# Performance work log

Hardware: AMD Instinct MI355X
Metric: run time of the kernel (lower is better)

Reference implementation:

```python
import jax, jax.numpy as jnp
import numpy as np

EPS = 1e-8


def setup_inputs() -> dict:
    key = jax.random.key(0)
    k1, = jax.random.split(key, 1)
    B, C, T = 8, 512, 16000
    x = jax.random.normal(k1, (B, C, T), dtype=jnp.float32)
    gamma = jnp.ones((1, C, 1), dtype=jnp.float32)
    beta = jnp.zeros((1, C, 1), dtype=jnp.float32)
    return {"x": x, "gamma": gamma, "beta": beta}


def reference(x, gamma, beta):
    # x: [B, C, T] cumulative layer norm (cLN)
    B, C, T = x.shape
    counts = C * (jnp.arange(T, dtype=x.dtype) + 1.0)  # [T], elements seen so far
    counts = counts.reshape(1, 1, T)
    # cumulative mean over (channels x time-so-far)
    mean = jnp.cumsum(x.sum(axis=1, keepdims=True), axis=2) / counts  # [B,1,T]
    # cumulative variance of residuals w.r.t. running mean (as in original)
    var = jnp.cumsum(((x - mean) ** 2).sum(axis=1, keepdims=True), axis=2) / counts  # [B,1,T]
    return (x - mean) / jnp.sqrt(var + EPS) * gamma + beta
```

## Files before the change

### kernel.cpp

```cpp
#include <hip/hip_runtime.h>
#include <hip/hip_bf16.h>


constexpr int Bb = 8;
constexpr int Cc = 512;
constexpr int Tt = 16000;
constexpr int T4 = Tt / 4;
constexpr int TCH = 128;
constexpr int T4CH = TCH / 4;
constexpr int NCHK = Tt / TCH;
constexpr float EPSF = 1e-8f;

typedef float f32x4 __attribute__((ext_vector_type(4)));

__device__ __forceinline__ unsigned long long pack_av(float v) {
    return (1ull << 32) | (unsigned long long)__float_as_uint(v);
}

__device__ __forceinline__ float lookback_sum(const unsigned long long* W,
                                              int chain_base, int k, int lane)
{
    float carry = 0.f;
    #pragma unroll 1
    for (int base = 0; base < k; base += 64) {
        const int j = base + lane;
        float v = 0.f;
        if (j < k) {
            unsigned long long w;
            for (;;) {
                w = __hip_atomic_load(&W[chain_base + j], __ATOMIC_RELAXED,
                                      __HIP_MEMORY_SCOPE_AGENT);
                if (w >> 32) break;
                __builtin_amdgcn_s_sleep(1);
            }
            v = __uint_as_float((unsigned)w);
        }
        #pragma unroll
        for (int m = 1; m < 64; m <<= 1) v += __shfl_xor(v, m, 64);
        carry += v;
    }
    return carry;
}

__global__ __launch_bounds__(1024)
void fused_cln_kernel(const float* __restrict__ x,
                      const float* __restrict__ gamma,
                      const float* __restrict__ beta,
                      float* __restrict__ out,
                      unsigned long long* __restrict__ W1,
                      unsigned long long* __restrict__ W2)
{
    const int bid = blockIdx.x;
    const int k = bid >> 3;
    const int b = bid & 7;
    const int tid = threadIdx.x;
    const int c_sub = tid >> 5;
    const int t4s   = tid & 31;

    __shared__ float gam[Cc], bet[Cc];
    if (tid < Cc) { gam[tid] = gamma[tid]; bet[tid] = beta[tid]; }

    const f32x4* xb = (const f32x4*)x + ((size_t)(b * Cc + c_sub)) * T4 + k * T4CH + t4s;
    f32x4 xr[16];
    #pragma unroll
    for (int r = 0; r < 16; ++r) xr[r] = xb[(size_t)r * 32 * T4];

    f32x4 ps = 0, pq = 0;
    #pragma unroll
    for (int r = 0; r < 16; ++r) { ps += xr[r]; pq += xr[r] * xr[r]; }

    __shared__ f32x4 red_s[32][32];
    __shared__ f32x4 red_q[32][32];
    red_s[c_sub][t4s] = ps;
    red_q[c_sub][t4s] = pq;
    __syncthreads();
    #pragma unroll
    for (int s = 16; s > 0; s >>= 1) {
        if (c_sub < s) {
            red_s[c_sub][t4s] += red_s[c_sub + s][t4s];
            red_q[c_sub][t4s] += red_q[c_sub + s][t4s];
        }
        __syncthreads();
    }

    __shared__ f32x4 mean_l[32], istd_l[32];

    if (tid < 64) {
        const int lane = tid;
        const bool act = lane < 32;
        const int chain = b * NCHK;

        const f32x4 sv = act ? red_s[0][lane] : (f32x4)0.f;
        const f32x4 qv = act ? red_q[0][lane] : (f32x4)0.f;

        const float c0 = sv.x, c1 = c0 + sv.y, c2 = c1 + sv.z, c3 = c2 + sv.w;
        float lsum = act ? c3 : 0.f;
        float sc = lsum;
        #pragma unroll
        for (int off = 1; off < 64; off <<= 1) {
            const float n = __shfl_up(sc, off, 64);
            if (lane >= off) sc += n;
        }
        const float total1 = __shfl(sc, 63, 64);
        const float ex1 = sc - lsum;

        if (lane == 0)
            __hip_atomic_store(&W1[chain + k], pack_av(total1), __ATOMIC_RELAXED,
                               __HIP_MEMORY_SCOPE_AGENT);
        const float carry1 = lookback_sum(W1, chain, k, lane);

        const float t0f = (float)(k * TCH + lane * 4);
        f32x4 cnt;
        cnt.x = (float)Cc * (t0f + 1.f);
        cnt.y = (float)Cc * (t0f + 2.f);
        cnt.z = (float)Cc * (t0f + 3.f);
        cnt.w = (float)Cc * (t0f + 4.f);

        f32x4 cs1;
        cs1.x = carry1 + ex1 + c0;
        cs1.y = carry1 + ex1 + c1;
        cs1.z = carry1 + ex1 + c2;
        cs1.w = carry1 + ex1 + c3;
        const f32x4 mn = cs1 / cnt;
        if (act) mean_l[lane] = mn;

        f32x4 s2 = qv - 2.f * mn * sv + (float)Cc * mn * mn;
        if (!act) s2 = 0.f;

        const float d0 = s2.x, d1 = d0 + s2.y, d2 = d1 + s2.z, d3 = d2 + s2.w;
        float lsum2 = act ? d3 : 0.f;
        float sc2 = lsum2;
        #pragma unroll
        for (int off = 1; off < 64; off <<= 1) {
            const float n = __shfl_up(sc2, off, 64);
            if (lane >= off) sc2 += n;
        }
        const float total2 = __shfl(sc2, 63, 64);
        const float ex2 = sc2 - lsum2;

        if (lane == 0)
            __hip_atomic_store(&W2[chain + k], pack_av(total2), __ATOMIC_RELAXED,
                               __HIP_MEMORY_SCOPE_AGENT);
        const float carry2 = lookback_sum(W2, chain, k, lane);

        if (act) {
            f32x4 cs2;
            cs2.x = carry2 + ex2 + d0;
            cs2.y = carry2 + ex2 + d1;
            cs2.z = carry2 + ex2 + d2;
            cs2.w = carry2 + ex2 + d3;
            const f32x4 var = cs2 / cnt;
            f32x4 is;
            is.x = rsqrtf(var.x + EPSF);
            is.y = rsqrtf(var.y + EPSF);
            is.z = rsqrtf(var.z + EPSF);
            is.w = rsqrtf(var.w + EPSF);
            istd_l[lane] = is;
        }
    }
    __syncthreads();

    const f32x4 m4 = mean_l[t4s];
    const f32x4 s4 = istd_l[t4s];
    f32x4* ob = (f32x4*)out + ((size_t)(b * Cc + c_sub)) * T4 + k * T4CH + t4s;
    #pragma unroll
    for (int r = 0; r < 16; ++r) {
        const int c = c_sub + 32 * r;
        const float g  = gam[c];
        const float be = bet[c];
        const f32x4 sg   = s4 * g;
        const f32x4 off4 = be - m4 * sg;
        __builtin_nontemporal_store(xr[r] * sg + off4, &ob[(size_t)r * 32 * T4]);
    }
}

extern "C" void kernel_launch(void* const* d_in, const int* in_sizes, int n_in,
                              void* d_out, int out_size, void* d_ws, size_t ws_size,
                              hipStream_t stream) {
    const float* x     = (const float*)d_in[0];
    const float* gamma = (const float*)d_in[1];
    const float* beta  = (const float*)d_in[2];
    float* out = (float*)d_out;

    unsigned long long* W1 = (unsigned long long*)d_ws;
    unsigned long long* W2 = W1 + (size_t)Bb * NCHK;

    hipMemsetAsync(d_ws, 0, 2 * (size_t)Bb * NCHK * sizeof(unsigned long long), stream);

    fused_cln_kernel<<<Bb * NCHK, 1024, 0, stream>>>(x, gamma, beta, out, W1, W2);
}
```

Measured before the change: 97.38 us.

## Shrink time chunks to 32, use 512-thread blocks with wave-shuffle reductions

```diff
diff --git a/kernel.cpp b/kernel.cpp
--- a/kernel.cpp
+++ b/kernel.cpp
@@ -6,7 +6,7 @@
 constexpr int Cc = 512;
 constexpr int Tt = 16000;
 constexpr int T4 = Tt / 4;
-constexpr int TCH = 128;
+constexpr int TCH = 32;
 constexpr int T4CH = TCH / 4;
 constexpr int NCHK = Tt / TCH;
 constexpr float EPSF = 1e-8f;
@@ -15,6 +15,15 @@
 
 __device__ __forceinline__ unsigned long long pack_av(float v) {
     return (1ull << 32) | (unsigned long long)__float_as_uint(v);
+}
+
+__device__ __forceinline__ f32x4 shflx(f32x4 v, int m) {
+    f32x4 r;
+    r.x = __shfl_xor(v.x, m, 64);
+    r.y = __shfl_xor(v.y, m, 64);
+    r.z = __shfl_xor(v.z, m, 64);
+    r.w = __shfl_xor(v.w, m, 64);
+    return r;
 }
 
 __device__ __forceinline__ float lookback_sum(const unsigned long long* W,
@@ -42,7 +51,7 @@
     return carry;
 }
 
-__global__ __launch_bounds__(1024)
+__global__ __launch_bounds__(512, 8)
 void fused_cln_kernel(const float* __restrict__ x,
                       const float* __restrict__ gamma,
                       const float* __restrict__ beta,
@@ -54,54 +63,51 @@
     const int k = bid >> 3;
     const int b = bid & 7;
     const int tid = threadIdx.x;
-    const int c_sub = tid >> 5;
-    const int t4s   = tid & 31;
+    const int c_sub = tid >> 3;
+    const int t4s   = tid & 7;
+    const int lane  = tid & 63;
+    const int wave  = tid >> 6;
 
     __shared__ float gam[Cc], bet[Cc];
-    if (tid < Cc) { gam[tid] = gamma[tid]; bet[tid] = beta[tid]; }
+    gam[tid] = gamma[tid];
+    bet[tid] = beta[tid];
 
-    const f32x4* xb = (const f32x4*)x + ((size_t)(b * Cc + c_sub)) * T4 + k * T4CH + t4s;
-    f32x4 xr[16];
+    const f32x4* xb = (const f32x4*)x + (size_t)(b * Cc + c_sub) * T4 + k * T4CH + t4s;
+    f32x4 xr[8];
     #pragma unroll
-    for (int r = 0; r < 16; ++r) xr[r] = xb[(size_t)r * 32 * T4];
+    for (int r = 0; r < 8; ++r) xr[r] = xb[(size_t)r * 64 * T4];
 
     f32x4 ps = 0, pq = 0;
     #pragma unroll
-    for (int r = 0; r < 16; ++r) { ps += xr[r]; pq += xr[r] * xr[r]; }
+    for (int r = 0; r < 8; ++r) { ps += xr[r]; pq += xr[r] * xr[r]; }
 
-    __shared__ f32x4 red_s[32][32];
-    __shared__ f32x4 red_q[32][32];
-    red_s[c_sub][t4s] = ps;
-    red_q[c_sub][t4s] = pq;
+    #pragma unroll
+    for (int m = 8; m < 64; m <<= 1) { ps += shflx(ps, m); pq += shflx(pq, m); }
+
+    __shared__ f32x4 red_s[8][8], red_q[8][8];
+    if (lane < 8) { red_s[wave][lane] = ps; red_q[wave][lane] = pq; }
     __syncthreads();
-    #pragma unroll
-    for (int s = 16; s > 0; s >>= 1) {
-        if (c_sub < s) {
-            red_s[c_sub][t4s] += red_s[c_sub + s][t4s];
-            red_q[c_sub][t4s] += red_q[c_sub + s][t4s];
-        }
-        __syncthreads();
-    }
 
-    __shared__ f32x4 mean_l[32], istd_l[32];
+    __shared__ f32x4 mean_l[8], istd_l[8];
 
     if (tid < 64) {
-        const int lane = tid;
-        const bool act = lane < 32;
+        f32x4 sv = red_s[lane >> 3][lane & 7];
+        f32x4 qv = red_q[lane >> 3][lane & 7];
+        #pragma unroll
+        for (int m = 8; m < 64; m <<= 1) { sv += shflx(sv, m); qv += shflx(qv, m); }
+
+        const bool act = lane < 8;
         const int chain = b * NCHK;
-
-        const f32x4 sv = act ? red_s[0][lane] : (f32x4)0.f;
-        const f32x4 qv = act ? red_q[0][lane] : (f32x4)0.f;
 
         const float c0 = sv.x, c1 = c0 + sv.y, c2 = c1 + sv.z, c3 = c2 + sv.w;
         float lsum = act ? c3 : 0.f;
         float sc = lsum;
         #pragma unroll
-        for (int off = 1; off < 64; off <<= 1) {
+        for (int off = 1; off < 8; off <<= 1) {
             const float n = __shfl_up(sc, off, 64);
             if (lane >= off) sc += n;
         }
-        const float total1 = __shfl(sc, 63, 64);
+        const float total1 = __shfl(sc, 7, 64);
         const float ex1 = sc - lsum;
 
         if (lane == 0)
@@ -131,11 +137,11 @@
         float lsum2 = act ? d3 : 0.f;
         float sc2 = lsum2;
         #pragma unroll
-        for (int off = 1; off < 64; off <<= 1) {
+        for (int off = 1; off < 8; off <<= 1) {
             const float n = __shfl_up(sc2, off, 64);
             if (lane >= off) sc2 += n;
         }
-        const float total2 = __shfl(sc2, 63, 64);
+        const float total2 = __shfl(sc2, 7, 64);
         const float ex2 = sc2 - lsum2;
 
         if (lane == 0)
@@ -162,15 +168,13 @@
 
     const f32x4 m4 = mean_l[t4s];
     const f32x4 s4 = istd_l[t4s];
-    f32x4* ob = (f32x4*)out + ((size_t)(b * Cc + c_sub)) * T4 + k * T4CH + t4s;
+    f32x4* ob = (f32x4*)out + (size_t)(b * Cc + c_sub) * T4 + k * T4CH + t4s;
     #pragma unroll
-    for (int r = 0; r < 16; ++r) {
-        const int c = c_sub + 32 * r;
-        const float g  = gam[c];
-        const float be = bet[c];
-        const f32x4 sg   = s4 * g;
-        const f32x4 off4 = be - m4 * sg;
-        __builtin_nontemporal_store(xr[r] * sg + off4, &ob[(size_t)r * 32 * T4]);
+    for (int r = 0; r < 8; ++r) {
+        const int c = c_sub + 64 * r;
+        const f32x4 sg   = s4 * gam[c];
+        const f32x4 off4 = bet[c] - m4 * sg;
+        __builtin_nontemporal_store(xr[r] * sg + off4, &ob[(size_t)r * 64 * T4]);
     }
 }
 
@@ -187,5 +191,5 @@
 
     hipMemsetAsync(d_ws, 0, 2 * (size_t)Bb * NCHK * sizeof(unsigned long long), stream);
 
-    fused_cln_kernel<<<Bb * NCHK, 1024, 0, stream>>>(x, gamma, beta, out, W1, W2);
+    fused_cln_kernel<<<Bb * NCHK, 512, 0, stream>>>(x, gamma, beta, out, W1, W2);
 }
```

Measured after the change: 126.5 us. 29.9% more time.
